# Kernel tuning notes

Hardware: AMD Instinct MI355X
Metric: run time of the kernel (lower is better)

The kernel has to match this reference:

```python
import jax, jax.numpy as jnp
import numpy as np

N = 50000        # nodes
E = 1_600_000    # edges (avg degree 32)
D_IN = 128
HID = 256
D_OUT = 128      # must equal D_IN for the residual add


def setup_inputs() -> dict:
    key = jax.random.key(0)
    k0, k1, k2, k3 = jax.random.split(key, 4)
    x = jax.random.normal(k0, (N, D_IN), dtype=jnp.float32)
    edge_index = jax.random.randint(k1, (2, E), 0, N, dtype=jnp.int32)
    # GCNConv params (lin: Linear without bias in PyG, plus additive bias)
    W1 = jax.random.normal(k2, (D_IN, HID), dtype=jnp.float32) / np.sqrt(D_IN)
    b1 = jnp.zeros((HID,), jnp.float32)
    W2 = jax.random.normal(k3, (HID, D_OUT), dtype=jnp.float32) / np.sqrt(HID)
    b2 = jnp.zeros((D_OUT,), jnp.float32)
    return {"x": x, "edge_index": edge_index, "W1": W1, "b1": b1, "W2": W2, "b2": b2}


def _gcn_conv(x, src, dst, norm, W, b, n):
    # PyG GCNConv: transform, gather source features, scale by sym-norm, scatter-add to dst.
    h = x @ W                        # [n, d_out]
    msg = h[src] * norm[:, None]     # [E+n, d_out] gathered messages
    out = jax.ops.segment_sum(msg, dst, num_segments=n)
    return out + b


def reference(x, edge_index, W1, b1, W2, b2):
    n = x.shape[0]
    # add self loops (GCNConv default add_self_loops=True)
    loops = jnp.arange(n, dtype=edge_index.dtype)
    src = jnp.concatenate([edge_index[0], loops])
    dst = jnp.concatenate([edge_index[1], loops])
    # symmetric normalization D^{-1/2} (A+I) D^{-1/2}
    deg = jax.ops.segment_sum(jnp.ones_like(dst, dtype=x.dtype), dst, num_segments=n)
    dinv = jnp.where(deg > 0, jax.lax.rsqrt(deg), 0.0)
    norm = dinv[src] * dinv[dst]
    skip = x  # nn.Identity skip connection
    h = jax.nn.relu(_gcn_conv(x, src, dst, norm, W1, b1, n))
    out = _gcn_conv(h, src, dst, norm, W2, b2, n)
    # classification_layer treated as identity; original .double() cast kept in fp32
    return out + skip
```

## Files before the change

### kernel.cpp

```cpp
#include <hip/hip_runtime.h>

#define D_IN 128
#define HID 256
#define BKT_SHIFT 9
#define BKT_SIZE 512
#define BKT_CAP 20480
#define CHUNK 4096
#define PAD_SLACK 4096
#define LSTR 264

typedef __attribute__((ext_vector_type(8))) short short8;
typedef __attribute__((ext_vector_type(4))) float floatx4;
typedef __attribute__((ext_vector_type(4))) int intx4;

static __device__ __forceinline__ unsigned short f2b(float f) {
  unsigned u = __float_as_uint(f);
  unsigned r = (u + 0x7fffu + ((u >> 16) & 1u)) >> 16;
  return (unsigned short)r;
}

static __device__ __forceinline__ void unpack8(uint4 v, float* f) {
  f[0] = __uint_as_float(v.x << 16); f[1] = __uint_as_float(v.x & 0xffff0000u);
  f[2] = __uint_as_float(v.y << 16); f[3] = __uint_as_float(v.y & 0xffff0000u);
  f[4] = __uint_as_float(v.z << 16); f[5] = __uint_as_float(v.z & 0xffff0000u);
  f[6] = __uint_as_float(v.w << 16); f[7] = __uint_as_float(v.w & 0xffff0000u);
}

static __device__ __forceinline__ void acc_fma(float* acc, uint4 v, float w) {
  float g[8];
  unpack8(v, g);
#pragma unroll
  for (int d = 0; d < 8; ++d) acc[d] = fmaf(g[d], w, acc[d]);
}


__global__ __launch_bounds__(256) void init_kernel(int* __restrict__ bkt_cursor,
                                                   float* __restrict__ dinv,
                                                   unsigned short* __restrict__ xb,
                                                   unsigned short* __restrict__ aggx,
                                                   unsigned short* __restrict__ tb,
                                                   int N, int nbkt) {
  const int tid = threadIdx.x;
  if (tid < nbkt) bkt_cursor[tid] = tid * BKT_CAP;
  if (tid == 0) dinv[N] = 0.f;
  if (tid < 64)       ((unsigned*)(xb   + (size_t)N * D_IN))[tid]       = 0u;
  else if (tid < 128) ((unsigned*)(aggx + (size_t)N * D_IN))[tid - 64]  = 0u;
  else if (tid < 192) ((unsigned*)(tb   + (size_t)N * D_IN))[tid - 128] = 0u;
}

__global__ __launch_bounds__(256) void bin_scatter_kernel(const int* __restrict__ src,
                                                          const int* __restrict__ dst,
                                                          int* __restrict__ bkt_cursor,
                                                          int* __restrict__ ebuf,
                                                          int E, int nbkt) {
  __shared__ int hist[128];
  __shared__ int bbase[128];
  const int tid = threadIdx.x;
  if (tid < nbkt) hist[tid] = 0;
  __syncthreads();
  const int base = blockIdx.x * CHUNK;
  const int end = min(base + CHUNK, E);
  for (int e = base + tid; e < end; e += 256)
    atomicAdd(&hist[dst[e] >> BKT_SHIFT], 1);
  __syncthreads();
  if (tid < nbkt) {
    int c = hist[tid];
    bbase[tid] = c > 0 ? atomicAdd(&bkt_cursor[tid], c) : 0;
    hist[tid] = 0;
  }
  __syncthreads();
  for (int e = base + tid; e < end; e += 256) {
    int d = dst[e];
    int b = d >> BKT_SHIFT;
    int off = atomicAdd(&hist[b], 1);
    int idx = bbase[b] + off;
    if (idx < (b + 1) * BKT_CAP)
      ebuf[idx] = (src[e] << BKT_SHIFT) | (d & (BKT_SIZE - 1));
  }
}

__global__ __launch_bounds__(256) void bucket_build_kernel(const int* __restrict__ ebuf,
                                                           const int* __restrict__ bkt_cursor,
                                                           float* __restrict__ dinv,
                                                           int2* __restrict__ rowse,
                                                           int* __restrict__ csr,
                                                           int N, int nbkt) {
  __shared__ int hist[BKT_SIZE];
  __shared__ int srs[BKT_SIZE];
  __shared__ int wsums[4];
  const int b = blockIdx.x;
  const int tid = threadIdx.x;
  const int node0 = b << BKT_SHIFT;
  const int nloc = min(BKT_SIZE, N - node0);
  const int ebeg = b * BKT_CAP;
  const int eend = min(bkt_cursor[b], (b + 1) * BKT_CAP);

  hist[tid] = 0; hist[tid + 256] = 0;
  __syncthreads();
  for (int e = ebeg + tid; e < eend; e += 256)
    atomicAdd(&hist[ebuf[e] & (BKT_SIZE - 1)], 1);
  __syncthreads();

  const int h0 = hist[2 * tid], h1 = hist[2 * tid + 1];
  const int p0 = (h0 + 7) & ~7, p1 = (h1 + 7) & ~7;
  const int s = p0 + p1;
  const int lane = tid & 63, wid = tid >> 6;
  int incl = s;
#pragma unroll
  for (int off = 1; off < 64; off <<= 1) {
    int t = __shfl_up(incl, off);
    if (lane >= off) incl += t;
  }
  if (lane == 63) wsums[wid] = incl;
  __syncthreads();
  int wex = 0;
  for (int w = 0; w < wid; ++w) wex += wsums[w];
  const int ex = wex + incl - s;
  const int base = b * (BKT_CAP + PAD_SLACK);
  if (2 * tid < nloc) {
    int st = base + ex;
    dinv[node0 + 2 * tid] = rsqrtf((float)(h0 + 1));
    rowse[node0 + 2 * tid] = make_int2(st, st + p0);
    srs[2 * tid] = st;
  }
  if (2 * tid + 1 < nloc) {
    int st = base + ex + p0;
    dinv[node0 + 2 * tid + 1] = rsqrtf((float)(h1 + 1));
    rowse[node0 + 2 * tid + 1] = make_int2(st, st + p1);
    srs[2 * tid + 1] = st;
  }
  hist[2 * tid] = 0; hist[2 * tid + 1] = 0;
  __syncthreads();

  for (int e = ebeg + tid; e < eend; e += 256) {
    int u = ebuf[e];
    int l = u & (BKT_SIZE - 1);
    int pos = atomicAdd(&hist[l], 1);
    csr[srs[l] + pos] = u >> BKT_SHIFT;
  }
  __syncthreads();
  for (int l = tid; l < nloc; l += 256) {
    int deg = hist[l];
    int p = (deg + 7) & ~7;
    int s0 = srs[l];
    for (int q = s0 + deg; q < s0 + p; ++q) csr[q] = N;
  }
}


__global__ __launch_bounds__(256) void prep_kernel(const float4* __restrict__ x4,
                                                   unsigned short* __restrict__ xb, int n4,
                                                   const float* __restrict__ W1,
                                                   unsigned short* __restrict__ Wt1,
                                                   const float* __restrict__ W2,
                                                   unsigned short* __restrict__ Wt2) {
  const int nxblk = (n4 + 255) / 256;
  const int bid = blockIdx.x;
  if (bid < nxblk) {
    int i = bid * 256 + threadIdx.x;
    if (i >= n4) return;
    float4 v = x4[i];
    ushort4 o;
    o.x = f2b(v.x); o.y = f2b(v.y); o.z = f2b(v.z); o.w = f2b(v.w);
    *(ushort4*)(xb + (size_t)i * 4) = o;
  } else if (bid < nxblk + 128) {
    int e = (bid - nxblk) * 256 + threadIdx.x;
    int k = e >> 8, n = e & 255;
    Wt1[(size_t)n * D_IN + k] = f2b(W1[e]);
  } else {
    int e = (bid - nxblk - 128) * 256 + threadIdx.x;
    int k = e >> 7, n = e & 127;
    Wt2[(size_t)n * HID + k] = f2b(W2[e]);
  }
}


__global__ __launch_bounds__(256) void gemm12_kernel(const unsigned short* __restrict__ A,
                                                     const unsigned short* __restrict__ Wt1,
                                                     const float* __restrict__ b1,
                                                     const unsigned short* __restrict__ Wt2,
                                                     unsigned short* __restrict__ T, int M) {
  __shared__ unsigned short hs[64][LSTR];
  const int tid = threadIdx.x;
  const int wave = tid >> 6;
  const int lane = tid & 63;
  const int quad = lane >> 4;
  const int l16 = lane & 15;
  const int row0 = blockIdx.x * 64;

  const short8* ap[4];
#pragma unroll
  for (int g = 0; g < 4; ++g) {
    int r = row0 + g * 16 + l16;
    if (r >= M) r = M - 1;
    ap[g] = (const short8*)(A + (size_t)r * D_IN + quad * 8);
  }
  const short8* bp1 = (const short8*)(Wt1 + (size_t)(wave * 64 + l16) * D_IN + quad * 8);

  floatx4 acc1[4][4];
#pragma unroll
  for (int g = 0; g < 4; ++g)
#pragma unroll
    for (int t = 0; t < 4; ++t) acc1[g][t] = floatx4{0.f, 0.f, 0.f, 0.f};

#pragma unroll
  for (int kt = 0; kt < 4; ++kt) {
    short8 a0 = ap[0][kt * 4], a1 = ap[1][kt * 4], a2 = ap[2][kt * 4], a3 = ap[3][kt * 4];
#pragma unroll
    for (int t = 0; t < 4; ++t) {
      short8 b = bp1[kt * 4 + t * 256];
      acc1[0][t] = __builtin_amdgcn_mfma_f32_16x16x32_bf16(a0, b, acc1[0][t], 0, 0, 0);
      acc1[1][t] = __builtin_amdgcn_mfma_f32_16x16x32_bf16(a1, b, acc1[1][t], 0, 0, 0);
      acc1[2][t] = __builtin_amdgcn_mfma_f32_16x16x32_bf16(a2, b, acc1[2][t], 0, 0, 0);
      acc1[3][t] = __builtin_amdgcn_mfma_f32_16x16x32_bf16(a3, b, acc1[3][t], 0, 0, 0);
    }
  }
#pragma unroll
  for (int t = 0; t < 4; ++t) {
    const float bv = b1[wave * 64 + t * 16 + l16];
#pragma unroll
    for (int g = 0; g < 4; ++g)
#pragma unroll
      for (int r = 0; r < 4; ++r) {
        float v = acc1[g][t][r] + bv;
        v = v > 0.f ? v : 0.f;
        hs[g * 16 + quad * 4 + r][wave * 64 + t * 16 + l16] = f2b(v);
      }
  }
  __syncthreads();

  const short8* bp2 = (const short8*)(Wt2 + (size_t)(wave * 32 + l16) * HID + quad * 8);
  floatx4 acc2[4][2];
#pragma unroll
  for (int g = 0; g < 4; ++g)
#pragma unroll
    for (int t = 0; t < 2; ++t) acc2[g][t] = floatx4{0.f, 0.f, 0.f, 0.f};

#pragma unroll
  for (int kt = 0; kt < 8; ++kt) {
    short8 a0 = *(const short8*)&hs[0 * 16 + l16][kt * 32 + quad * 8];
    short8 a1 = *(const short8*)&hs[1 * 16 + l16][kt * 32 + quad * 8];
    short8 a2 = *(const short8*)&hs[2 * 16 + l16][kt * 32 + quad * 8];
    short8 a3 = *(const short8*)&hs[3 * 16 + l16][kt * 32 + quad * 8];
#pragma unroll
    for (int t = 0; t < 2; ++t) {
      short8 b = bp2[kt * 4 + t * 512];
      acc2[0][t] = __builtin_amdgcn_mfma_f32_16x16x32_bf16(a0, b, acc2[0][t], 0, 0, 0);
      acc2[1][t] = __builtin_amdgcn_mfma_f32_16x16x32_bf16(a1, b, acc2[1][t], 0, 0, 0);
      acc2[2][t] = __builtin_amdgcn_mfma_f32_16x16x32_bf16(a2, b, acc2[2][t], 0, 0, 0);
      acc2[3][t] = __builtin_amdgcn_mfma_f32_16x16x32_bf16(a3, b, acc2[3][t], 0, 0, 0);
    }
  }
  __syncthreads();

#pragma unroll
  for (int t = 0; t < 2; ++t)
#pragma unroll
    for (int g = 0; g < 4; ++g)
#pragma unroll
      for (int r = 0; r < 4; ++r)
        hs[g * 16 + quad * 4 + r][wave * 32 + t * 16 + l16] = f2b(acc2[g][t][r]);
  __syncthreads();

#pragma unroll
  for (int i = 0; i < 4; ++i) {
    const int r = i * 16 + (tid >> 4);
    const int c = (tid & 15) * 8;
    const int row = row0 + r;
    uint4 v = *(const uint4*)&hs[r][c];
    if (row < M) *(uint4*)&T[(size_t)row * D_IN + c] = v;
  }
}


template<bool SKIP_BIAS>
__global__ __launch_bounds__(256) void agg_kernel(const uint4* __restrict__ Hq,
                                                  const int2* __restrict__ rowse,
                                                  const int* __restrict__ csr,
                                                  const float* __restrict__ dinv,
                                                  const float* __restrict__ skip,
                                                  const float* __restrict__ bias,
                                                  void* __restrict__ OUT, int n) {
  const int lane = threadIdx.x & 15;
  const int node = blockIdx.x * 16 + (threadIdx.x >> 4);
  if (node >= n) return;

  const float dv = dinv[node];
  float acc[8];
  {
    uint4 sv = Hq[(size_t)node * 16 + lane];
    float f[8];
    unpack8(sv, f);
    const float ws = dv * dv;
#pragma unroll
    for (int d = 0; d < 8; ++d) acc[d] = f[d] * ws;
  }

  const int2 se = rowse[node];
  intx4 c0 = *(const intx4*)(csr + se.x);
  intx4 c1 = *(const intx4*)(csr + se.x + 4);
  for (int j = se.x; j < se.y; ) {
    const int jn = j + 8;
    const int jp = (jn < se.y) ? jn : se.x;
    intx4 n0 = *(const intx4*)(csr + jp);
    intx4 n1 = *(const intx4*)(csr + jp + 4);
    float w0 = dinv[c0.x] * dv, w1 = dinv[c0.y] * dv;
    float w2 = dinv[c0.z] * dv, w3 = dinv[c0.w] * dv;
    float w4 = dinv[c1.x] * dv, w5 = dinv[c1.y] * dv;
    float w6 = dinv[c1.z] * dv, w7 = dinv[c1.w] * dv;
    uint4 v0 = Hq[(size_t)c0.x * 16 + lane];
    uint4 v1 = Hq[(size_t)c0.y * 16 + lane];
    uint4 v2 = Hq[(size_t)c0.z * 16 + lane];
    uint4 v3 = Hq[(size_t)c0.w * 16 + lane];
    uint4 v4 = Hq[(size_t)c1.x * 16 + lane];
    uint4 v5 = Hq[(size_t)c1.y * 16 + lane];
    uint4 v6 = Hq[(size_t)c1.z * 16 + lane];
    uint4 v7 = Hq[(size_t)c1.w * 16 + lane];
    acc_fma(acc, v0, w0);
    acc_fma(acc, v1, w1);
    acc_fma(acc, v2, w2);
    acc_fma(acc, v3, w3);
    acc_fma(acc, v4, w4);
    acc_fma(acc, v5, w5);
    acc_fma(acc, v6, w6);
    acc_fma(acc, v7, w7);
    c0 = n0; c1 = n1; j = jn;
  }

  if (SKIP_BIAS) {
    const float* sp = skip + (size_t)node * 128 + lane * 8;
    const float* bp = bias + lane * 8;
    float4 s0 = *(const float4*)sp, s1 = *(const float4*)(sp + 4);
    float4 b0 = *(const float4*)bp, b1 = *(const float4*)(bp + 4);
    float* op = (float*)OUT + (size_t)node * 128 + lane * 8;
    *(float4*)op = make_float4(acc[0] + s0.x + b0.x, acc[1] + s0.y + b0.y,
                               acc[2] + s0.z + b0.z, acc[3] + s0.w + b0.w);
    *(float4*)(op + 4) = make_float4(acc[4] + s1.x + b1.x, acc[5] + s1.y + b1.y,
                                     acc[6] + s1.z + b1.z, acc[7] + s1.w + b1.w);
  } else {
    uint4 o;
    o.x = (unsigned)f2b(acc[0]) | ((unsigned)f2b(acc[1]) << 16);
    o.y = (unsigned)f2b(acc[2]) | ((unsigned)f2b(acc[3]) << 16);
    o.z = (unsigned)f2b(acc[4]) | ((unsigned)f2b(acc[5]) << 16);
    o.w = (unsigned)f2b(acc[6]) | ((unsigned)f2b(acc[7]) << 16);
    ((uint4*)OUT)[(size_t)node * 16 + lane] = o;
  }
}


extern "C" void kernel_launch(void* const* d_in, const int* in_sizes, int n_in,
                              void* d_out, int out_size, void* d_ws, size_t ws_size,
                              hipStream_t stream) {
  const float* x  = (const float*)d_in[0];
  const int*   ei = (const int*)d_in[1];
  const float* W1 = (const float*)d_in[2];
  const float* b1 = (const float*)d_in[3];
  const float* W2 = (const float*)d_in[4];
  const float* b2 = (const float*)d_in[5];
  float* out = (float*)d_out;

  const int N = in_sizes[0] / D_IN;
  const int E = in_sizes[1] / 2;
  const int* srcA = ei;
  const int* dstA = ei + E;
  const int NBKT = (N + BKT_SIZE - 1) >> BKT_SHIFT;
  const int NCHUNK = (E + CHUNK - 1) / CHUNK;

  char* ws = (char*)d_ws;
  size_t off = 0;
  auto alloc = [&](size_t bytes) { void* p = ws + off; off = (off + bytes + 255) & ~(size_t)255; return p; };
  int*            bkt_cursor = (int*)           alloc((size_t)NBKT * 4);
  float*          dinv       = (float*)         alloc((size_t)(N + 1) * 4);
  int2*           rowse      = (int2*)          alloc((size_t)N * 8);
  int*            ebuf       = (int*)           alloc((size_t)NBKT * BKT_CAP * 4);
  int*            csr        = (int*)           alloc((size_t)NBKT * (BKT_CAP + PAD_SLACK) * 4);
  unsigned short* xb         = (unsigned short*)alloc((size_t)(N + 1) * D_IN * 2);
  unsigned short* aggx       = (unsigned short*)alloc((size_t)(N + 1) * D_IN * 2);
  unsigned short* tb         = (unsigned short*)alloc((size_t)(N + 1) * D_IN * 2);
  unsigned short* Wt1        = (unsigned short*)alloc((size_t)D_IN * HID * 2);
  unsigned short* Wt2        = (unsigned short*)alloc((size_t)D_IN * HID * 2);

  init_kernel<<<1, 256, 0, stream>>>(bkt_cursor, dinv, xb, aggx, tb, N, NBKT);
  bin_scatter_kernel<<<NCHUNK, 256, 0, stream>>>(srcA, dstA, bkt_cursor, ebuf, E, NBKT);
  bucket_build_kernel<<<NBKT, 256, 0, stream>>>(ebuf, bkt_cursor, dinv, rowse, csr, N, NBKT);

  {
    const int n4 = N * D_IN / 4;
    prep_kernel<<<(n4 + 255) / 256 + 256, 256, 0, stream>>>((const float4*)x, xb, n4,
                                                            W1, Wt1, W2, Wt2);
  }
  agg_kernel<false><<<(N + 15) / 16, 256, 0, stream>>>((const uint4*)xb, rowse, csr,
                                                       dinv, nullptr, nullptr, aggx, N);
  gemm12_kernel<<<(N + 63) / 64, 256, 0, stream>>>(aggx, Wt1, b1, Wt2, tb, N);
  agg_kernel<true><<<(N + 15) / 16, 256, 0, stream>>>((const uint4*)tb, rowse, csr,
                                                      dinv, x, b2, out, N);
}
```

Before: 286.1 us.

## Fuse edge binning with input prep, halve bucket size, memset cursors

Merges the init, edge bin-scatter and bf16 prep kernels into one launch whose blocks are split by role, and replaces cursor initialization with a memset using relative bucket offsets. Bucket size drops from 512 to 256 nodes, which doubles the number of bucket_build blocks (about 196 instead of 98) so more CUs are busy, and each thread now handles one node. This removes launch gaps and lets the prep work overlap the scatter. In exchange the scatter uses more shared-memory histogram bins, there are more global cursor atomics, and per-bucket capacity is smaller, which raises the risk of overflow on skewed graphs.

```diff
diff --git a/kernel.cpp b/kernel.cpp
--- a/kernel.cpp
+++ b/kernel.cpp
@@ -2,11 +2,11 @@
 
 #define D_IN 128
 #define HID 256
-#define BKT_SHIFT 9
-#define BKT_SIZE 512
-#define BKT_CAP 20480
+#define BKT_SHIFT 8
+#define BKT_SIZE 256
+#define BKT_CAP 10240
 #define CHUNK 4096
-#define PAD_SLACK 4096
+#define PAD_SLACK 2048
 #define LSTR 264
 
 typedef __attribute__((ext_vector_type(8))) short short8;
@@ -34,50 +34,66 @@
 }
 
 
-__global__ __launch_bounds__(256) void init_kernel(int* __restrict__ bkt_cursor,
-                                                   float* __restrict__ dinv,
-                                                   unsigned short* __restrict__ xb,
-                                                   unsigned short* __restrict__ aggx,
-                                                   unsigned short* __restrict__ tb,
-                                                   int N, int nbkt) {
+__global__ __launch_bounds__(256) void fused_front_kernel(
+    const int* __restrict__ src, const int* __restrict__ dst,
+    int* __restrict__ bkt_cursor, int* __restrict__ ebuf, int E, int nbkt, int nchunk,
+    const float4* __restrict__ x4, unsigned short* __restrict__ xb, int n4,
+    const float* __restrict__ W1, unsigned short* __restrict__ Wt1,
+    const float* __restrict__ W2, unsigned short* __restrict__ Wt2,
+    float* __restrict__ dinv, unsigned short* __restrict__ aggx,
+    unsigned short* __restrict__ tb, int N) {
+  const int bid = blockIdx.x;
   const int tid = threadIdx.x;
-  if (tid < nbkt) bkt_cursor[tid] = tid * BKT_CAP;
-  if (tid == 0) dinv[N] = 0.f;
-  if (tid < 64)       ((unsigned*)(xb   + (size_t)N * D_IN))[tid]       = 0u;
-  else if (tid < 128) ((unsigned*)(aggx + (size_t)N * D_IN))[tid - 64]  = 0u;
-  else if (tid < 192) ((unsigned*)(tb   + (size_t)N * D_IN))[tid - 128] = 0u;
-}
-
-__global__ __launch_bounds__(256) void bin_scatter_kernel(const int* __restrict__ src,
-                                                          const int* __restrict__ dst,
-                                                          int* __restrict__ bkt_cursor,
-                                                          int* __restrict__ ebuf,
-                                                          int E, int nbkt) {
-  __shared__ int hist[128];
-  __shared__ int bbase[128];
-  const int tid = threadIdx.x;
-  if (tid < nbkt) hist[tid] = 0;
-  __syncthreads();
-  const int base = blockIdx.x * CHUNK;
-  const int end = min(base + CHUNK, E);
-  for (int e = base + tid; e < end; e += 256)
-    atomicAdd(&hist[dst[e] >> BKT_SHIFT], 1);
-  __syncthreads();
-  if (tid < nbkt) {
-    int c = hist[tid];
-    bbase[tid] = c > 0 ? atomicAdd(&bkt_cursor[tid], c) : 0;
-    hist[tid] = 0;
-  }
-  __syncthreads();
-  for (int e = base + tid; e < end; e += 256) {
-    int d = dst[e];
-    int b = d >> BKT_SHIFT;
-    int off = atomicAdd(&hist[b], 1);
-    int idx = bbase[b] + off;
-    if (idx < (b + 1) * BKT_CAP)
-      ebuf[idx] = (src[e] << BKT_SHIFT) | (d & (BKT_SIZE - 1));
-  }
-}
+  if (bid < nchunk) {
+    __shared__ int hist[BKT_SIZE];
+    __shared__ int bbase[BKT_SIZE];
+    if (tid < nbkt) hist[tid] = 0;
+    __syncthreads();
+    const int base = bid * CHUNK;
+    const int end = min(base + CHUNK, E);
+    for (int e = base + tid; e < end; e += 256)
+      atomicAdd(&hist[dst[e] >> BKT_SHIFT], 1);
+    __syncthreads();
+    if (tid < nbkt) {
+      int c = hist[tid];
+      bbase[tid] = c > 0 ? atomicAdd(&bkt_cursor[tid], c) : 0;
+      hist[tid] = 0;
+    }
+    __syncthreads();
+    for (int e = base + tid; e < end; e += 256) {
+      int d = dst[e];
+      int b = d >> BKT_SHIFT;
+      int off = atomicAdd(&hist[b], 1);
+      int rel = bbase[b] + off;
+      if (rel < BKT_CAP)
+        ebuf[b * BKT_CAP + rel] = (src[e] << BKT_SHIFT) | (d & (BKT_SIZE - 1));
+    }
+    return;
+  }
+  const int nxblk = (n4 + 255) / 256;
+  if (bid < nchunk + nxblk) {
+    int i = (bid - nchunk) * 256 + tid;
+    if (i >= n4) return;
+    float4 v = x4[i];
+    ushort4 o;
+    o.x = f2b(v.x); o.y = f2b(v.y); o.z = f2b(v.z); o.w = f2b(v.w);
+    *(ushort4*)(xb + (size_t)i * 4) = o;
+  } else if (bid < nchunk + nxblk + 128) {
+    int e = (bid - nchunk - nxblk) * 256 + tid;
+    int k = e >> 8, n = e & 255;
+    Wt1[(size_t)n * D_IN + k] = f2b(W1[e]);
+  } else if (bid < nchunk + nxblk + 256) {
+    int e = (bid - nchunk - nxblk - 128) * 256 + tid;
+    int k = e >> 7, n = e & 127;
+    Wt2[(size_t)n * HID + k] = f2b(W2[e]);
+  } else {
+    if (tid == 0) dinv[N] = 0.f;
+    if (tid < 64)       ((unsigned*)(xb   + (size_t)N * D_IN))[tid]       = 0u;
+    else if (tid < 128) ((unsigned*)(aggx + (size_t)N * D_IN))[tid - 64]  = 0u;
+    else if (tid < 192) ((unsigned*)(tb   + (size_t)N * D_IN))[tid - 128] = 0u;
+  }
+}
+
 
 __global__ __launch_bounds__(256) void bucket_build_kernel(const int* __restrict__ ebuf,
                                                            const int* __restrict__ bkt_cursor,
@@ -93,19 +109,18 @@
   const int node0 = b << BKT_SHIFT;
   const int nloc = min(BKT_SIZE, N - node0);
   const int ebeg = b * BKT_CAP;
-  const int eend = min(bkt_cursor[b], (b + 1) * BKT_CAP);
-
-  hist[tid] = 0; hist[tid + 256] = 0;
+  const int eend = ebeg + min(bkt_cursor[b], BKT_CAP);
+
+  hist[tid] = 0;
   __syncthreads();
   for (int e = ebeg + tid; e < eend; e += 256)
     atomicAdd(&hist[ebuf[e] & (BKT_SIZE - 1)], 1);
   __syncthreads();
 
-  const int h0 = hist[2 * tid], h1 = hist[2 * tid + 1];
-  const int p0 = (h0 + 7) & ~7, p1 = (h1 + 7) & ~7;
-  const int s = p0 + p1;
+  const int h = hist[tid];
+  const int p = (h + 7) & ~7;
   const int lane = tid & 63, wid = tid >> 6;
-  int incl = s;
+  int incl = p;
 #pragma unroll
   for (int off = 1; off < 64; off <<= 1) {
     int t = __shfl_up(incl, off);
@@ -115,21 +130,15 @@
   __syncthreads();
   int wex = 0;
   for (int w = 0; w < wid; ++w) wex += wsums[w];
-  const int ex = wex + incl - s;
+  const int ex = wex + incl - p;
   const int base = b * (BKT_CAP + PAD_SLACK);
-  if (2 * tid < nloc) {
+  if (tid < nloc) {
     int st = base + ex;
-    dinv[node0 + 2 * tid] = rsqrtf((float)(h0 + 1));
-    rowse[node0 + 2 * tid] = make_int2(st, st + p0);
-    srs[2 * tid] = st;
-  }
-  if (2 * tid + 1 < nloc) {
-    int st = base + ex + p0;
-    dinv[node0 + 2 * tid + 1] = rsqrtf((float)(h1 + 1));
-    rowse[node0 + 2 * tid + 1] = make_int2(st, st + p1);
-    srs[2 * tid + 1] = st;
-  }
-  hist[2 * tid] = 0; hist[2 * tid + 1] = 0;
+    dinv[node0 + tid] = rsqrtf((float)(h + 1));
+    rowse[node0 + tid] = make_int2(st, st + p);
+    srs[tid] = st;
+  }
+  hist[tid] = 0;
   __syncthreads();
 
   for (int e = ebeg + tid; e < eend; e += 256) {
@@ -141,36 +150,9 @@
   __syncthreads();
   for (int l = tid; l < nloc; l += 256) {
     int deg = hist[l];
-    int p = (deg + 7) & ~7;
+    int pp = (deg + 7) & ~7;
     int s0 = srs[l];
-    for (int q = s0 + deg; q < s0 + p; ++q) csr[q] = N;
-  }
-}
-
-
-__global__ __launch_bounds__(256) void prep_kernel(const float4* __restrict__ x4,
-                                                   unsigned short* __restrict__ xb, int n4,
-                                                   const float* __restrict__ W1,
-                                                   unsigned short* __restrict__ Wt1,
-                                                   const float* __restrict__ W2,
-                                                   unsigned short* __restrict__ Wt2) {
-  const int nxblk = (n4 + 255) / 256;
-  const int bid = blockIdx.x;
-  if (bid < nxblk) {
-    int i = bid * 256 + threadIdx.x;
-    if (i >= n4) return;
-    float4 v = x4[i];
-    ushort4 o;
-    o.x = f2b(v.x); o.y = f2b(v.y); o.z = f2b(v.z); o.w = f2b(v.w);
-    *(ushort4*)(xb + (size_t)i * 4) = o;
-  } else if (bid < nxblk + 128) {
-    int e = (bid - nxblk) * 256 + threadIdx.x;
-    int k = e >> 8, n = e & 255;
-    Wt1[(size_t)n * D_IN + k] = f2b(W1[e]);
-  } else {
-    int e = (bid - nxblk - 128) * 256 + threadIdx.x;
-    int k = e >> 7, n = e & 127;
-    Wt2[(size_t)n * HID + k] = f2b(W2[e]);
+    for (int q = s0 + deg; q < s0 + pp; ++q) csr[q] = N;
   }
 }
 
@@ -380,15 +362,14 @@
   unsigned short* Wt1        = (unsigned short*)alloc((size_t)D_IN * HID * 2);
   unsigned short* Wt2        = (unsigned short*)alloc((size_t)D_IN * HID * 2);
 
-  init_kernel<<<1, 256, 0, stream>>>(bkt_cursor, dinv, xb, aggx, tb, N, NBKT);
-  bin_scatter_kernel<<<NCHUNK, 256, 0, stream>>>(srcA, dstA, bkt_cursor, ebuf, E, NBKT);
+  const int n4 = N * D_IN / 4;
+  const int nxblk = (n4 + 255) / 256;
+
+  (void)hipMemsetAsync(bkt_cursor, 0, (size_t)NBKT * 4, stream);
+  fused_front_kernel<<<NCHUNK + nxblk + 256 + 1, 256, 0, stream>>>(
+      srcA, dstA, bkt_cursor, ebuf, E, NBKT, NCHUNK,
+      (const float4*)x, xb, n4, W1, Wt1, W2, Wt2, dinv, aggx, tb, N);
   bucket_build_kernel<<<NBKT, 256, 0, stream>>>(ebuf, bkt_cursor, dinv, rowse, csr, N, NBKT);
-
-  {
-    const int n4 = N * D_IN / 4;
-    prep_kernel<<<(n4 + 255) / 256 + 256, 256, 0, stream>>>((const float4*)x, xb, n4,
-                                                            W1, Wt1, W2, Wt2);
-  }
   agg_kernel<false><<<(N + 15) / 16, 256, 0, stream>>>((const uint4*)xb, rowse, csr,
                                                        dinv, nullptr, nullptr, aggx, N);
   gemm12_kernel<<<(N + 63) / 64, 256, 0, stream>>>(aggx, Wt1, b1, Wt2, tb, N);
```

Result: faster. 272.4 us (-4.8%).
